# Kernel optimization log

Measured on AMD Instinct MI355X. Metric: run time of the kernel, lower is better.

The kernel has to match this reference:

```python
import jax, jax.numpy as jnp
import numpy as np
import math

N_HEADS = 16


def setup_inputs() -> dict:
    key = jax.random.key(0)
    ks = jax.random.split(key, 6)
    B, S, D = 2, 2048, 2048
    hd = D // N_HEADS  # 128
    scale = 0.02
    x = jax.random.normal(ks[0], (B, S, D), dtype=jnp.float32)
    wq = jax.random.normal(ks[1], (D, D), dtype=jnp.float32) * scale
    wk = jax.random.normal(ks[2], (D, D), dtype=jnp.float32) * scale
    wv = jax.random.normal(ks[3], (D, D), dtype=jnp.float32) * scale
    wo = jax.random.normal(ks[4], (D, D), dtype=jnp.float32) * scale
    # Rotary frequencies: theta = 10000^(-2i/hd), angle[t, i] = t * theta_i
    inv_freq = 1.0 / (10000.0 ** (jnp.arange(0, hd, 2, dtype=jnp.float32) / hd))  # [hd//2]
    angles = jnp.arange(S, dtype=jnp.float32)[:, None] * inv_freq[None, :]  # [S, hd//2]
    freqs_cos = jnp.cos(angles)
    freqs_sin = jnp.sin(angles)
    # Causal additive mask [1,1,S,S]
    causal = jnp.tril(jnp.ones((S, S), dtype=bool))
    mask = jnp.where(causal, 0.0, -1e9).astype(jnp.float32)[None, None]
    return {"x": x, "wq": wq, "wk": wk, "wv": wv, "wo": wo,
            "freqs_cos": freqs_cos, "freqs_sin": freqs_sin, "mask": mask}


def _apply_rope(t, cos, sin):
    # t: [B,S,H,hd]; cos/sin: [S, hd//2]. Complex mult on (even, odd) pairs.
    B, S, H, hd = t.shape
    tr = t.reshape(B, S, H, hd // 2, 2)
    t0, t1 = tr[..., 0], tr[..., 1]
    c = cos[None, :, None, :]
    s = sin[None, :, None, :]
    o0 = t0 * c - t1 * s
    o1 = t0 * s + t1 * c
    return jnp.stack([o0, o1], axis=-1).reshape(B, S, H, hd)


def reference(x, wq, wk, wv, wo, freqs_cos, freqs_sin, mask):
    B, S, D = x.shape
    H = N_HEADS
    hd = D // H
    # Projections (torch Linear: y = x @ W^T)
    q = jnp.einsum('bsd,ed->bse', x, wq).reshape(B, S, H, hd)
    k = jnp.einsum('bsd,ed->bse', x, wk).reshape(B, S, H, hd)
    v = jnp.einsum('bsd,ed->bse', x, wv).reshape(B, S, H, hd)
    q = _apply_rope(q, freqs_cos, freqs_sin)
    k = _apply_rope(k, freqs_cos, freqs_sin)
    # Attention: scores [B,H,S,S]
    scores = jnp.einsum('bshd,bthd->bhst', q, k) / math.sqrt(hd)
    scores = scores + mask[:, :, :S, :S]
    attn = jax.nn.softmax(scores.astype(jnp.float32), axis=-1).astype(q.dtype)
    out = jnp.einsum('bhst,bthd->bshd', attn, v).reshape(B, S, D)
    return jnp.einsum('bsd,ed->bse', out, wo)
```

## Files before the change

### kernel.cpp

```cpp
#include <hip/hip_runtime.h>

typedef unsigned short u16;
typedef __attribute__((ext_vector_type(8))) short short8;
typedef __attribute__((ext_vector_type(4))) short short4s;
typedef __attribute__((ext_vector_type(4))) float f32x4;

__device__ __forceinline__ u16 f2b(float f) {
  union { float f; unsigned u; } c; c.f = f;
  unsigned u = c.u;
  unsigned r = (u + 0x7FFFu + ((u >> 16) & 1u)) >> 16;
  return (u16)r;
}
__device__ __forceinline__ float b2f(u16 h) {
  union { unsigned u; float f; } c; c.u = ((unsigned)h) << 16;
  return c.f;
}

__device__ __forceinline__ void gload16(const u16* g, u16* l) {
  __builtin_amdgcn_global_load_lds((const __attribute__((address_space(1))) void*)g,
                                   (__attribute__((address_space(3))) void*)l, 16, 0, 0);
}

__device__ __forceinline__ short4s tr16(const u16* p) {
  short4s d;
  asm volatile("ds_read_b64_tr_b16 %0, %1"
               : "=v"(d)
               : "v"((const __attribute__((address_space(3))) u16*)p));
  return d;
}

#define MFMA(a, b, c) __builtin_amdgcn_mfma_f32_16x16x32_bf16(a, b, c, 0, 0, 0)

__global__ __launch_bounds__(256) void cast_all(const float* __restrict__ x,
                                                const float* __restrict__ wq,
                                                const float* __restrict__ wk,
                                                const float* __restrict__ wv,
                                                const float* __restrict__ wo,
                                                u16* __restrict__ xb,
                                                u16* __restrict__ wqkv,
                                                u16* __restrict__ wob) {
  int i = blockIdx.x * 256 + threadIdx.x;
  const float4* s; u16* d; int off;
  if (i < 2097152)      { s = (const float4*)x;  d = xb;            off = i; }
  else if (i < 3145728) { s = (const float4*)wq; d = wqkv;          off = i - 2097152; }
  else if (i < 4194304) { s = (const float4*)wk; d = wqkv + 4194304; off = i - 3145728; }
  else if (i < 5242880) { s = (const float4*)wv; d = wqkv + 8388608; off = i - 4194304; }
  else                  { s = (const float4*)wo; d = wob;           off = i - 5242880; }
  float4 v = s[off];
  ushort4 r;
  r.x = f2b(v.x); r.y = f2b(v.y); r.z = f2b(v.z); r.w = f2b(v.w);
  *(ushort4*)(d + (size_t)off * 4) = r;
}

__global__ __launch_bounds__(256) void rope_k(u16* __restrict__ qkv,
                                              const float* __restrict__ fc,
                                              const float* __restrict__ fs) {
  int idx = blockIdx.x * 256 + threadIdx.x;
  int m = idx >> 8;
  int c = idx & 255;
  int s = m & 2047;
  int i0 = (c * 4) & 63;
  u16* p = qkv + (size_t)m * 6144 + 2048 + c * 8;
  short8 v = *(short8*)p;
  float4 cs = *(const float4*)(fc + (size_t)s * 64 + i0);
  float4 sn = *(const float4*)(fs + (size_t)s * 64 + i0);
  float cc[4] = {cs.x, cs.y, cs.z, cs.w};
  float ss[4] = {sn.x, sn.y, sn.z, sn.w};
#pragma unroll
  for (int t = 0; t < 4; ++t) {
    float x0 = b2f((u16)v[2 * t]);
    float x1 = b2f((u16)v[2 * t + 1]);
    float o0 = x0 * cc[t] - x1 * ss[t];
    float o1 = x0 * ss[t] + x1 * cc[t];
    v[2 * t]     = (short)f2b(o0);
    v[2 * t + 1] = (short)f2b(o1);
  }
  *(short8*)p = v;
}

template <int NREP, int F32OUT>
__global__ __launch_bounds__(512, 2) void gemm_big(const u16* __restrict__ Ag,
                                                   const u16* __restrict__ Bg,
                                                   void* __restrict__ Cp,
                                                   int M, int N, int K) {
  __shared__ __align__(16) u16 lds[32768 + NREP * 8192];
  const int tid = threadIdx.x;
  const int l = tid & 63, w = tid >> 6;
  const int wm = w >> 2, wn = w & 3;
  const int ln = l & 15, lk = l >> 4;
  const int BN = NREP * 64;
  const int nbn = N / BN;
  const int nwg = (M >> 8) * nbn;
  const int wg = ((blockIdx.x & 7) * (nwg >> 3)) + (blockIdx.x >> 3);
  const int row0 = (wg / nbn) << 8;
  const int col0 = (wg % nbn) * BN;
  const int T = K >> 6;

#define STAGE_A(t, h)                                                                  \
  {                                                                                    \
    _Pragma("unroll")                                                                  \
    for (int u = 0; u < 2; ++u) {                                                      \
      int e = u * 512 + tid;                                                           \
      int rr = (h) * 128 + (e >> 3);                                                   \
      gload16(Ag + (size_t)(row0 + rr) * K + (t) * 64 + (((e & 7) ^ (rr & 7)) << 3),   \
              lds + ((t) & 1) * 16384 + (h) * 8192 + e * 8);                           \
    }                                                                                  \
  }
#define STAGE_B(t, pb)                                                                 \
  {                                                                                    \
    int rr = (pb) * 64 + (tid >> 3);                                                   \
    gload16(Bg + (size_t)(col0 + rr) * K + (t) * 64 + (((tid & 7) ^ (rr & 7)) << 3),   \
            lds + 32768 + ((t) & 1) * NREP * 4096 + (pb) * 4096 + tid * 8);            \
  }

  f32x4 acc[8][NREP];
#pragma unroll
  for (int m = 0; m < 8; ++m)
#pragma unroll
    for (int n = 0; n < NREP; ++n) acc[m][n] = (f32x4){0.f, 0.f, 0.f, 0.f};

  const int x = ln & 7;
  const int c0 = (lk ^ x) << 3;
  const int c1 = ((4 + lk) ^ x) << 3;

#pragma unroll
  for (int pb = 0; pb < NREP; ++pb) STAGE_B(0, pb);
  STAGE_A(0, 0); STAGE_A(0, 1);
#pragma unroll
  for (int pb = 0; pb < NREP; ++pb) STAGE_B(1, pb);
  if (NREP == 3) { asm volatile("s_waitcnt vmcnt(3)" ::: "memory"); }
  else           { asm volatile("s_waitcnt vmcnt(2)" ::: "memory"); }
  __builtin_amdgcn_s_barrier();

  for (int t = 0; t < T; ++t) {
    const u16* aB = lds + (t & 1) * 16384 + wm * 8192;
    const u16* bB = lds + 32768 + (t & 1) * NREP * 4096;
    short8 bf[NREP][2];
#pragma unroll
    for (int p = 0; p < 4; ++p) {
      if (p == 0) {
#pragma unroll
        for (int n = 0; n < NREP; ++n) {
          int rb = (wn * NREP * 16 + n * 16 + ln) * 64;
          bf[n][0] = *(const short8*)&bB[rb + c0];
          bf[n][1] = *(const short8*)&bB[rb + c1];
        }
      }
      short8 af[2][2];
#pragma unroll
      for (int m2 = 0; m2 < 2; ++m2) {
        int ra = ((p * 2 + m2) * 16 + ln) * 64;
        af[m2][0] = *(const short8*)&aB[ra + c0];
        af[m2][1] = *(const short8*)&aB[ra + c1];
      }
      if (p == 0)      { if (t + 1 < T) STAGE_A(t + 1, 0); }
      else if (p == 1) { if (t + 1 < T) STAGE_A(t + 1, 1);
                         if (t + 2 < T) STAGE_B(t + 2, 0); }
      else if (p == 2) { if (t + 2 < T) STAGE_B(t + 2, 1); }
      else             { if (NREP == 3 && t + 2 < T) STAGE_B(t + 2, 2); }

      __builtin_amdgcn_s_setprio(1);
#pragma unroll
      for (int m2 = 0; m2 < 2; ++m2)
#pragma unroll
        for (int n = 0; n < NREP; ++n)
#pragma unroll
          for (int kk = 0; kk < 2; ++kk)
            acc[p * 2 + m2][n] = MFMA(af[m2][kk], bf[n][kk], acc[p * 2 + m2][n]);
      __builtin_amdgcn_s_setprio(0);

      if (p == 3) {
        if (t + 2 < T) {
          if (NREP == 3) { asm volatile("s_waitcnt vmcnt(3)" ::: "memory"); }
          else           { asm volatile("s_waitcnt vmcnt(2)" ::: "memory"); }
        } else if (t + 1 < T) {
          asm volatile("s_waitcnt vmcnt(0)" ::: "memory");
        }
      }
      __builtin_amdgcn_s_barrier();
    }
  }

#pragma unroll
  for (int m = 0; m < 8; ++m) {
    int r0 = row0 + wm * 128 + m * 16 + lk * 4;
#pragma unroll
    for (int n = 0; n < NREP; ++n) {
      int cc = col0 + wn * NREP * 16 + n * 16 + ln;
#pragma unroll
      for (int j = 0; j < 4; ++j) {
        float v = acc[m][n][j];
        if (F32OUT) ((float*)Cp)[(size_t)(r0 + j) * N + cc] = v;
        else        ((u16*)Cp)[(size_t)(r0 + j) * N + cc]   = f2b(v);
      }
    }
  }
#undef STAGE_A
#undef STAGE_B
}

__global__ __launch_bounds__(512) void attn_fwd(const u16* __restrict__ qkv,
                                                const float* __restrict__ fc,
                                                const float* __restrict__ fs,
                                                u16* __restrict__ out) {
  __shared__ __align__(16) u16 sK[2][64 * 128];
  __shared__ __align__(16) u16 sV[2][64 * 128];
  __shared__ __align__(16) u16 sP[8][16 * 72];
  const int tid = threadIdx.x, l = tid & 63, w = tid >> 6;
  const int ln = l & 15, lk = l >> 4;

  const int bid = blockIdx.x;
  const int l0 = ((bid & 7) << 5) | (bid >> 3);
  const int bh = l0 >> 3, pr = l0 & 7;
  const int b = bh >> 4, h = bh & 15;

  const u16* Kp = qkv + (size_t)b * 2048 * 6144 + 2048 + h * 128;
  const u16* Vp = Kp + 2048;
  const float scale = 0.08838834764831845f;

  for (int pass = 0; pass < 2; ++pass) {
    const int qt = pass ? (15 - pr) : pr;
    const int m0 = b * 2048 + qt * 128;
    const u16* Qp = qkv + (size_t)m0 * 6144 + h * 128;
    const int srow = qt * 128 + w * 16 + ln;

    short8 qf[4];
#pragma unroll
    for (int kc = 0; kc < 4; ++kc) {
      short8 raw = *(const short8*)(Qp + (size_t)(w * 16 + ln) * 6144 + kc * 32 + lk * 8);
      float4 c4 = *(const float4*)(fc + (size_t)srow * 64 + kc * 16 + lk * 4);
      float4 s4 = *(const float4*)(fs + (size_t)srow * 64 + kc * 16 + lk * 4);
      float cc[4] = {c4.x * scale, c4.y * scale, c4.z * scale, c4.w * scale};
      float ss[4] = {s4.x * scale, s4.y * scale, s4.z * scale, s4.w * scale};
#pragma unroll
      for (int t = 0; t < 4; ++t) {
        float x0 = b2f((u16)raw[2 * t]);
        float x1 = b2f((u16)raw[2 * t + 1]);
        qf[kc][2 * t]     = (short)f2b(x0 * cc[t] - x1 * ss[t]);
        qf[kc][2 * t + 1] = (short)f2b(x0 * ss[t] + x1 * cc[t]);
      }
    }

    f32x4 o[8];
#pragma unroll
    for (int d = 0; d < 8; ++d) o[d] = (f32x4){0.f, 0.f, 0.f, 0.f};
    float mrow[4] = {-1e9f, -1e9f, -1e9f, -1e9f};
    float lsum[4] = {0.f, 0.f, 0.f, 0.f};

    const int ntl = 2 * qt + 2;

    {
#pragma unroll
      for (int q = 0; q < 2; ++q) {
        int e = q * 512 + tid;
        int r = e >> 4, p = e & 15;
        gload16(Kp + (size_t)r * 6144 + ((p ^ (r & 7)) << 3), &sK[0][e * 8]);
        int j = ((e >> 6) << 2) + ((e & 7) >> 1);
        int d = (((e >> 3) & 7) << 4) + ((e & 1) << 3);
        gload16(Vp + (size_t)j * 6144 + d, &sV[0][e * 8]);
      }
    }
    __syncthreads();

    int cur = 0;
    for (int jt = 0; jt < ntl; ++jt) {
      if (jt + 1 < ntl) {
        const u16* Kt = Kp + (size_t)(jt + 1) * 64 * 6144;
        const u16* Vt = Vp + (size_t)(jt + 1) * 64 * 6144;
        int nb = cur ^ 1;
#pragma unroll
        for (int q = 0; q < 2; ++q) {
          int e = q * 512 + tid;
          int r = e >> 4, p = e & 15;
          gload16(Kt + (size_t)r * 6144 + ((p ^ (r & 7)) << 3), &sK[nb][e * 8]);
          int j = ((e >> 6) << 2) + ((e & 7) >> 1);
          int d = (((e >> 3) & 7) << 4) + ((e & 1) << 3);
          gload16(Vt + (size_t)j * 6144 + d, &sV[nb][e * 8]);
        }
      }

      f32x4 sf[4];
      __builtin_amdgcn_s_setprio(1);
#pragma unroll
      for (int nc = 0; nc < 4; ++nc) {
        f32x4 s = (f32x4){0.f, 0.f, 0.f, 0.f};
#pragma unroll
        for (int kc = 0; kc < 4; ++kc) {
          int r = nc * 16 + ln;
          short8 kb = *(const short8*)&sK[cur][r * 128 + (((kc << 2) + lk) ^ (r & 7)) * 8];
          s = MFMA(qf[kc], kb, s);
        }
        sf[nc] = s;
      }
      __builtin_amdgcn_s_setprio(0);

      if (jt >= 2 * qt) {
        int ig = qt * 128 + w * 16 + lk * 4;
#pragma unroll
        for (int nc = 0; nc < 4; ++nc) {
          int jg = jt * 64 + nc * 16 + ln;
#pragma unroll
          for (int j = 0; j < 4; ++j)
            sf[nc][j] = (jg > ig + j) ? -1e9f : sf[nc][j];
        }
      }

      float tm[4];
#pragma unroll
      for (int j = 0; j < 4; ++j)
        tm[j] = fmaxf(fmaxf(sf[0][j], sf[1][j]), fmaxf(sf[2][j], sf[3][j]));
      int ok = (tm[0] <= mrow[0] + 8.f) & (tm[1] <= mrow[1] + 8.f) &
               (tm[2] <= mrow[2] + 8.f) & (tm[3] <= mrow[3] + 8.f);
      if (!__all(ok)) {
#pragma unroll
        for (int off = 1; off < 16; off <<= 1)
#pragma unroll
          for (int j = 0; j < 4; ++j) tm[j] = fmaxf(tm[j], __shfl_xor(tm[j], off, 16));
        float al[4];
#pragma unroll
        for (int j = 0; j < 4; ++j) {
          float nm = fmaxf(mrow[j], tm[j]);
          al[j] = __expf(mrow[j] - nm);
          mrow[j] = nm;
        }
#pragma unroll
        for (int d = 0; d < 8; ++d)
#pragma unroll
          for (int j = 0; j < 4; ++j) o[d][j] *= al[j];
#pragma unroll
        for (int j = 0; j < 4; ++j) lsum[j] *= al[j];
      }

#pragma unroll
      for (int nc = 0; nc < 4; ++nc)
#pragma unroll
        for (int j = 0; j < 4; ++j) {
          float p = __expf(sf[nc][j] - mrow[j]);
          u16 pb = f2b(p);
          sP[w][(lk * 4 + j) * 72 + nc * 16 + ln] = pb;
          lsum[j] += b2f(pb);
        }

      short8 pa0 = *(const short8*)&sP[w][ln * 72 + lk * 8];
      short8 pa1 = *(const short8*)&sP[w][ln * 72 + 32 + lk * 8];
      asm volatile("s_waitcnt lgkmcnt(0)" ::: "memory");
      __builtin_amdgcn_sched_barrier(0);

      short4s tb[4][4];
#define TRISSUE(dblk, slot)                                                  \
      {                                                                      \
        const u16* vb = &sV[cur][(lk * 2) * 512 + (dblk) * 64 + ln * 4];     \
        tb[slot][0] = tr16(vb);                                              \
        tb[slot][1] = tr16(vb + 512);                                        \
        tb[slot][2] = tr16(vb + 4096);                                       \
        tb[slot][3] = tr16(vb + 4096 + 512);                                 \
      }
      TRISSUE(0, 0);
      TRISSUE(1, 1);
      __builtin_amdgcn_s_setprio(1);
#pragma unroll
      for (int d = 0; d < 8; ++d) {
        if (d < 6) TRISSUE(d + 2, (d + 2) & 3);
        if (d < 6)       asm volatile("s_waitcnt lgkmcnt(8)" ::: "memory");
        else if (d == 6) asm volatile("s_waitcnt lgkmcnt(4)" ::: "memory");
        else             asm volatile("s_waitcnt lgkmcnt(0)" ::: "memory");
        __builtin_amdgcn_sched_barrier(0);
        short8 vb0 = {tb[d & 3][0][0], tb[d & 3][0][1], tb[d & 3][0][2], tb[d & 3][0][3],
                      tb[d & 3][1][0], tb[d & 3][1][1], tb[d & 3][1][2], tb[d & 3][1][3]};
        short8 vb1 = {tb[d & 3][2][0], tb[d & 3][2][1], tb[d & 3][2][2], tb[d & 3][2][3],
                      tb[d & 3][3][0], tb[d & 3][3][1], tb[d & 3][3][2], tb[d & 3][3][3]};
        o[d] = MFMA(pa0, vb0, o[d]);
        o[d] = MFMA(pa1, vb1, o[d]);
      }
      __builtin_amdgcn_s_setprio(0);
#undef TRISSUE

      __syncthreads();
      cur ^= 1;
    }

#pragma unroll
    for (int off = 1; off < 16; off <<= 1)
#pragma unroll
      for (int j = 0; j < 4; ++j) lsum[j] += __shfl_xor(lsum[j], off, 16);
    float inv[4];
#pragma unroll
    for (int j = 0; j < 4; ++j) inv[j] = 1.f / lsum[j];
#pragma unroll
    for (int d = 0; d < 8; ++d)
#pragma unroll
      for (int j = 0; j < 4; ++j)
        out[(size_t)(m0 + w * 16 + lk * 4 + j) * 2048 + h * 128 + d * 16 + ln] =
            f2b(o[d][j] * inv[j]);
  }
}

extern "C" void kernel_launch(void* const* d_in, const int* in_sizes, int n_in,
                              void* d_out, int out_size, void* d_ws, size_t ws_size,
                              hipStream_t stream) {
  const float* x  = (const float*)d_in[0];
  const float* wq = (const float*)d_in[1];
  const float* wk = (const float*)d_in[2];
  const float* wv = (const float*)d_in[3];
  const float* wo = (const float*)d_in[4];
  const float* fc = (const float*)d_in[5];
  const float* fs = (const float*)d_in[6];

  char* ws = (char*)d_ws;
  u16* xb   = (u16*)(ws);
  u16* wqkv = (u16*)(ws + 16777216);
  u16* wob  = (u16*)(ws + 41943040);
  u16* qkv  = (u16*)(ws + 50331648);
  u16* aout = (u16*)(ws + 100663296);

  cast_all<<<24576, 256, 0, stream>>>(x, wq, wk, wv, wo, xb, wqkv, wob);
  gemm_big<3, 0><<<512, 512, 0, stream>>>(xb, wqkv, qkv, 4096, 6144, 2048);
  rope_k<<<4096, 256, 0, stream>>>(qkv, fc, fs);
  attn_fwd<<<256, 512, 0, stream>>>(qkv, fc, fs, aout);
  gemm_big<2, 1><<<256, 512, 0, stream>>>(aout, wob, d_out, 4096, 2048, 2048);
}
```

Before: 249.8 us.

## Add wide 256x384 GEMM kernel with BK=32 for QKV projection

Adds a new GEMM kernel that uses a 256x384 output tile with a K-step of 32 and a different XOR swizzle, and uses it for the fused QKV projection. The grid drops from 512 to 256 workgroups, which raises per-block arithmetic intensity and fits one wave of CUs. The gemm_big template is simplified to drop its NREP==3 paths, since it is now only used for the output projection. The cost is 48 accumulator tiles per thread, which raises register pressure, and half as many K-steps of work between each barrier.

```diff
diff --git a/kernel.cpp b/kernel.cpp
--- a/kernel.cpp
+++ b/kernel.cpp
@@ -78,6 +78,114 @@
   *(short8*)p = v;
 }
 
+template <int F32OUT>
+__global__ __launch_bounds__(512, 2) void gemm_wide(const u16* __restrict__ Ag,
+                                                    const u16* __restrict__ Bg,
+                                                    void* __restrict__ Cp,
+                                                    int M, int N, int K) {
+  __shared__ __align__(16) u16 lds[40960];
+  const int tid = threadIdx.x;
+  const int l = tid & 63, w = tid >> 6;
+  const int wm = w >> 2, wn = w & 3;
+  const int ln = l & 15, lk = l >> 4;
+  const int nbn = N / 384;
+  const int nwg = (M >> 8) * nbn;
+  const int wg = ((blockIdx.x & 7) * (nwg >> 3)) + (blockIdx.x >> 3);
+  const int row0 = (wg / nbn) << 8;
+  const int col0 = (wg % nbn) * 384;
+  const int T = K >> 5;
+
+#define STAGE_A(t)                                                                     \
+  {                                                                                    \
+    _Pragma("unroll")                                                                  \
+    for (int u = 0; u < 2; ++u) {                                                      \
+      int e = u * 512 + tid;                                                           \
+      int rr = e >> 2;                                                                 \
+      gload16(Ag + (size_t)(row0 + rr) * K + (t) * 32 +                                \
+                  (((e & 3) ^ ((rr >> 1) & 3)) << 3),                                  \
+              lds + ((t) & 1) * 8192 + e * 8);                                         \
+    }                                                                                  \
+  }
+#define STAGE_B(t)                                                                     \
+  {                                                                                    \
+    _Pragma("unroll")                                                                  \
+    for (int u = 0; u < 3; ++u) {                                                      \
+      int e = u * 512 + tid;                                                           \
+      int rr = e >> 2;                                                                 \
+      gload16(Bg + (size_t)(col0 + rr) * K + (t) * 32 +                                \
+                  (((e & 3) ^ ((rr >> 1) & 3)) << 3),                                  \
+              lds + 16384 + ((t) & 1) * 12288 + e * 8);                                \
+    }                                                                                  \
+  }
+
+  f32x4 acc[8][6];
+#pragma unroll
+  for (int m = 0; m < 8; ++m)
+#pragma unroll
+    for (int n = 0; n < 6; ++n) acc[m][n] = (f32x4){0.f, 0.f, 0.f, 0.f};
+
+  const int cx = (lk ^ ((ln >> 1) & 3)) << 3;
+
+  STAGE_B(0); STAGE_A(0); STAGE_B(1);
+  asm volatile("s_waitcnt vmcnt(3)" ::: "memory");
+  __builtin_amdgcn_s_barrier();
+
+  for (int t = 0; t < T; ++t) {
+    const u16* aB = lds + (t & 1) * 8192;
+    const u16* bB = lds + 16384 + (t & 1) * 12288;
+    short8 bf[6];
+    short8 af[4];
+
+#pragma unroll
+    for (int n = 0; n < 6; ++n)
+      bf[n] = *(const short8*)&bB[(wn * 96 + n * 16 + ln) * 32 + cx];
+#pragma unroll
+    for (int mf = 0; mf < 4; ++mf)
+      af[mf] = *(const short8*)&aB[(wm * 128 + mf * 16 + ln) * 32 + cx];
+    if (t + 1 < T) STAGE_A(t + 1);
+    __builtin_amdgcn_s_setprio(1);
+#pragma unroll
+    for (int mf = 0; mf < 4; ++mf)
+#pragma unroll
+      for (int n = 0; n < 6; ++n)
+        acc[mf][n] = MFMA(af[mf], bf[n], acc[mf][n]);
+    __builtin_amdgcn_s_setprio(0);
+    __builtin_amdgcn_s_barrier();
+
+#pragma unroll
+    for (int mf = 0; mf < 4; ++mf)
+      af[mf] = *(const short8*)&aB[(wm * 128 + (4 + mf) * 16 + ln) * 32 + cx];
+    if (t + 2 < T) STAGE_B(t + 2);
+    __builtin_amdgcn_s_setprio(1);
+#pragma unroll
+    for (int mf = 0; mf < 4; ++mf)
+#pragma unroll
+      for (int n = 0; n < 6; ++n)
+        acc[4 + mf][n] = MFMA(af[mf], bf[n], acc[4 + mf][n]);
+    __builtin_amdgcn_s_setprio(0);
+    if (t + 2 < T) { asm volatile("s_waitcnt vmcnt(3)" ::: "memory"); }
+    else           { asm volatile("s_waitcnt vmcnt(0)" ::: "memory"); }
+    __builtin_amdgcn_s_barrier();
+  }
+
+#pragma unroll
+  for (int m = 0; m < 8; ++m) {
+    int r0 = row0 + wm * 128 + m * 16 + lk * 4;
+#pragma unroll
+    for (int n = 0; n < 6; ++n) {
+      int cc = col0 + wn * 96 + n * 16 + ln;
+#pragma unroll
+      for (int j = 0; j < 4; ++j) {
+        float v = acc[m][n][j];
+        if (F32OUT) ((float*)Cp)[(size_t)(r0 + j) * N + cc] = v;
+        else        ((u16*)Cp)[(size_t)(r0 + j) * N + cc]   = f2b(v);
+      }
+    }
+  }
+#undef STAGE_A
+#undef STAGE_B
+}
+
 template <int NREP, int F32OUT>
 __global__ __launch_bounds__(512, 2) void gemm_big(const u16* __restrict__ Ag,
                                                    const u16* __restrict__ Bg,
@@ -128,8 +236,7 @@
   STAGE_A(0, 0); STAGE_A(0, 1);
 #pragma unroll
   for (int pb = 0; pb < NREP; ++pb) STAGE_B(1, pb);
-  if (NREP == 3) { asm volatile("s_waitcnt vmcnt(3)" ::: "memory"); }
-  else           { asm volatile("s_waitcnt vmcnt(2)" ::: "memory"); }
+  asm volatile("s_waitcnt vmcnt(2)" ::: "memory");
   __builtin_amdgcn_s_barrier();
 
   for (int t = 0; t < T; ++t) {
@@ -157,7 +264,6 @@
       else if (p == 1) { if (t + 1 < T) STAGE_A(t + 1, 1);
                          if (t + 2 < T) STAGE_B(t + 2, 0); }
       else if (p == 2) { if (t + 2 < T) STAGE_B(t + 2, 1); }
-      else             { if (NREP == 3 && t + 2 < T) STAGE_B(t + 2, 2); }
 
       __builtin_amdgcn_s_setprio(1);
 #pragma unroll
@@ -170,12 +276,8 @@
       __builtin_amdgcn_s_setprio(0);
 
       if (p == 3) {
-        if (t + 2 < T) {
-          if (NREP == 3) { asm volatile("s_waitcnt vmcnt(3)" ::: "memory"); }
-          else           { asm volatile("s_waitcnt vmcnt(2)" ::: "memory"); }
-        } else if (t + 1 < T) {
-          asm volatile("s_waitcnt vmcnt(0)" ::: "memory");
-        }
+        if (t + 2 < T)      { asm volatile("s_waitcnt vmcnt(2)" ::: "memory"); }
+        else if (t + 1 < T) { asm volatile("s_waitcnt vmcnt(0)" ::: "memory"); }
       }
       __builtin_amdgcn_s_barrier();
     }
@@ -414,7 +516,7 @@
   u16* aout = (u16*)(ws + 100663296);
 
   cast_all<<<24576, 256, 0, stream>>>(x, wq, wk, wv, wo, xb, wqkv, wob);
-  gemm_big<3, 0><<<512, 512, 0, stream>>>(xb, wqkv, qkv, 4096, 6144, 2048);
+  gemm_wide<0><<<256, 512, 0, stream>>>(xb, wqkv, qkv, 4096, 6144, 2048);
   rope_k<<<4096, 256, 0, stream>>>(qkv, fc, fs);
   attn_fwd<<<256, 512, 0, stream>>>(qkv, fc, fs, aout);
   gemm_big<2, 1><<<256, 512, 0, stream>>>(aout, wob, d_out, 4096, 2048, 2048);
```

After: 239.8 us. 1.04x faster.
